# Optimization experiments

Measured on AMD Instinct MI355X. Metric: run time of the kernel, lower is better.

Reference implementation:

```python
import jax, jax.numpy as jnp
import numpy as np

KS = 5
NF = 64
B, H, W = 2, 160, 160


def _conv1x1(x, w, b):
    # x: (B,Ci,H,W), w: (Co,Ci)
    return jnp.einsum('oi,bihw->bohw', w, x) + b[None, :, None, None]


def _conv2x2(x, w, b, dil):
    # x: (B,1,Hp,Wp), w: (64,1,2,2); VALID conv with dilation dil
    y = jax.lax.conv_general_dilated(x, w, (1, 1), 'VALID',
                                     rhs_dilation=(dil, dil),
                                     dimension_numbers=('NCHW', 'OIHW', 'NCHW'))
    return y + b[None, :, None, None]


def _conv_s(x, w, b):
    # conv1 module, mode 's': gather taps (0,0),(1,1),(1,2),(2,1) of each 3x3 patch,
    # then (1,4) conv == linear combo of 4 shifted images.
    h = x.shape[2] - 2
    wd = x.shape[3] - 2
    x0 = x[:, 0]
    taps = jnp.stack([x0[:, 0:h, 0:wd],
                      x0[:, 1:h + 1, 1:wd + 1],
                      x0[:, 1:h + 1, 2:wd + 2],
                      x0[:, 2:h + 2, 1:wd + 1]], axis=1)  # (B,4,h,wd)
    return jnp.einsum('ok,bkhw->bohw', w.reshape(NF, 4), taps) + b[None, :, None, None]


def _construct(c, dense_ps):
    # relu then dense 1x1-conv chain with channel concat, final 1x1 -> 4 channels
    x = jax.nn.relu(c)
    for (wt, bs) in dense_ps[:-1]:
        feat = jax.nn.relu(_conv1x1(x, wt, bs))
        x = jnp.concatenate([x, feat], axis=1)
    wt, bs = dense_ps[-1]
    return _conv1x1(x, wt, bs)


def _ag(x, sigx, sigy, theta, sigr):
    # x: (B,ks,ks,HW); params: (B,HW). Per-pixel anisotropic bilateral kernel.
    ks = x.shape[1]
    r = jnp.arange(ks, dtype=x.dtype) - ks // 2
    sq = (r[:, None] ** 2 + r[None, :] ** 2)[None, :, :, None]  # (1,ks,ks,1)
    sx = sigx[:, None, None, :]
    sy = sigy[:, None, None, :]
    th = theta[:, None, None, :]
    sr = sigr[:, None, None, :]
    spatial = jnp.exp(-sq / (2.0 * sr ** 2))
    disx = jnp.abs(x[:, ks // 2:ks // 2 + 1] - x)       # center row
    disy = jnp.abs(x[:, :, ks // 2:ks // 2 + 1] - x)    # center col
    a = sx * disx
    bb = sy * disy
    color = jnp.exp(-0.5 * (a ** 2 - 2.0 * th * a * bb + bb ** 2))
    kern = spatial * color
    kern = kern / jnp.sum(kern, axis=(1, 2), keepdims=True)
    return jnp.sum(kern * x, axis=(1, 2))  # (B,HW)


def _forward(x_in, conv1x_w, conv1x_b, conv1c_w, conv1c_b, conv1cs_w, conv1cs_b,
             w2, b2, w3, b3, w4, b4, w5, b5, w6, b6):
    dense_ps = [(w2, b2), (w3, b3), (w4, b4), (w5, b5), (w6, b6)]

    def fk(x, mod):
        if mod == 's':
            c = _conv_s(x, conv1cs_w, conv1cs_b)
        elif mod == 'c':
            c = _conv2x2(x, conv1c_w, conv1c_b, 2)
        else:
            c = _conv2x2(x, conv1x_w, conv1x_b, 1)
        return _construct(c, dense_ps)

    def mode_ens(x, p, mod):
        pad = lambda z: jnp.pad(z, ((0, 0), (0, 0), (0, p), (0, p)), mode='reflect')
        r0 = fk(pad(x), mod)
        r2 = jnp.rot90(fk(pad(jnp.rot90(x, 2, (2, 3))), mod), 2, (2, 3))
        r1 = jnp.rot90(fk(pad(jnp.rot90(x, 1, (2, 3))), mod), 3, (2, 3))
        r3 = jnp.rot90(fk(pad(jnp.rot90(x, 3, (2, 3))), mod), 1, (2, 3))
        return (r0 + r2) / 2.0, (r1 + r3) / 2.0

    e1x, e2x = mode_ens(x_in, 1, 'x')
    e1s, e2s = mode_ens(x_in, 2, 's')
    e1c, e2c = mode_ens(x_in, 2, 'c')
    par = (e1x + e2x + e1s + e2s + e1c + e2c) / 6.0  # (B,4,H,W)

    b, c, h, w = x_in.shape
    sigx = jnp.clip(jax.nn.sigmoid(par[:, 0]).reshape(b, -1) + 1e-6, 0.0, 1.0)
    sigy = jnp.clip(jax.nn.sigmoid(par[:, 1]).reshape(b, -1) + 1e-6, 0.0, 1.0)
    theta = jnp.clip(jnp.tanh(par[:, 2]).reshape(b, -1), -1.0, 1.0)
    sigr = jnp.clip(jnp.tanh(par[:, 3]).reshape(b, -1) + 1e-6, -1.0, 1.0)

    ph = KS // 2
    xt = jnp.pad(x_in, ((0, 0), (0, 0), (ph, ph), (ph, ph)))  # zero pad
    # unfold -> (B, KS, KS, H*W)
    patches = jnp.stack([jnp.stack([xt[:, 0, i:i + h, j:j + w].reshape(b, -1)
                                    for j in range(KS)], axis=1)
                         for i in range(KS)], axis=1)
    outs = _ag(patches, sigx * 20.0, sigy * 20.0, theta, sigr * 10.0 + 10.0).reshape(b, c, h, w)
    return outs, sigx, sigy, theta, sigr


def setup_inputs() -> dict:
    key = jax.random.key(0)
    k = jax.random.split(key, 10)
    def kn(kk, shape, fan_in):
        return jax.random.normal(kk, shape, jnp.float32) * np.float32(np.sqrt(2.0 / fan_in))
    zb = lambda n: jnp.zeros((n,), jnp.float32)
    return {
        'x_in': jax.random.normal(k[0], (B, 1, H, W), jnp.float32),
        'conv1x_w': kn(k[1], (NF, 1, 2, 2), 4), 'conv1x_b': zb(NF),
        'conv1c_w': kn(k[2], (NF, 1, 2, 2), 4), 'conv1c_b': zb(NF),
        'conv1cs_w': kn(k[3], (NF, 1, 1, 4), 4), 'conv1cs_b': zb(NF),
        'w2': kn(k[4], (NF, NF), NF), 'b2': zb(NF),
        'w3': kn(k[5], (NF, 2 * NF), 2 * NF), 'b3': zb(NF),
        'w4': kn(k[6], (NF, 3 * NF), 3 * NF), 'b4': zb(NF),
        'w5': kn(k[7], (NF, 4 * NF), 4 * NF), 'b5': zb(NF),
        'w6': kn(k[8], (4, 5 * NF), 5 * NF), 'b6': zb(4),
    }


def reference(x_in, conv1x_w, conv1x_b, conv1c_w, conv1c_b, conv1cs_w, conv1cs_b,
              w2, b2, w3, b3, w4, b4, w5, b5, w6, b6):
    return _forward(x_in, conv1x_w, conv1x_b, conv1c_w, conv1c_b, conv1cs_w, conv1cs_b,
                    w2, b2, w3, b3, w4, b4, w5, b5, w6, b6)
```

## Files before the change

kernel.cpp:

```cpp
#include <hip/hip_runtime.h>
#include <hip/hip_bf16.h>
#include <math.h>
#include <string.h>


#define NN   160
#define NPIX 25600

typedef __attribute__((ext_vector_type(4))) float float4v;
typedef __attribute__((ext_vector_type(8))) unsigned short ushort8;
typedef __attribute__((ext_vector_type(2))) unsigned int uint2v;
typedef __attribute__((ext_vector_type(4))) unsigned int uint4v;
typedef __attribute__((ext_vector_type(8))) __bf16 bf16x8;

__device__ __forceinline__ int refp(int a) { return (a <= NN - 1) ? a : (2 * (NN - 1) - a); }

__device__ __forceinline__ unsigned int pk2(float lo, float hi) {
    float2 f; f.x = lo; f.y = hi;
    __hip_bfloat162 h = __float22bfloat162_rn(f);
    unsigned int u;
    memcpy(&u, &h, 4);
    return u;
}
__device__ __forceinline__ ushort8 cvt8(const float* __restrict__ p) {
    const float4v f0 = *(const float4v*)p;
    const float4v f1 = *(const float4v*)(p + 4);
    uint4v u;
    u[0] = pk2(f0[0], f0[1]); u[1] = pk2(f0[2], f0[3]);
    u[2] = pk2(f1[0], f1[1]); u[3] = pk2(f1[2], f1[3]);
    return __builtin_bit_cast(ushort8, u);
}

template <int NCH>
__device__ __forceinline__ void dense_layer(const ushort8 (&A)[NCH], float4v biasv,
                                            unsigned short* Xs, int w, int lo16, int lq) {
    const int K = NCH * 32;
#pragma unroll
    for (int pp = 0; pp < 2; ++pp) {
        const int px0 = (pp * 2) * 16 + lo16;
        const int px1 = (pp * 2 + 1) * 16 + lo16;
        float4v acc0 = biasv, acc1 = biasv;
#pragma unroll
        for (int s = 0; s < NCH; ++s) {
            const int c8 = s * 4 + lq;
            const bf16x8 bf0 = __builtin_bit_cast(bf16x8, *(const ushort8*)&Xs[c8 * 512 + px0 * 8]);
            const bf16x8 bf1 = __builtin_bit_cast(bf16x8, *(const ushort8*)&Xs[c8 * 512 + px1 * 8]);
            const bf16x8 af  = __builtin_bit_cast(bf16x8, A[s]);
            acc0 = __builtin_amdgcn_mfma_f32_16x16x32_bf16(af, bf0, acc0, 0, 0, 0);
            acc1 = __builtin_amdgcn_mfma_f32_16x16x32_bf16(af, bf1, acc1, 0, 0, 0);
        }
        const int cb = K + w * 16 + lq * 4;
        uint2v o0, o1;
        o0[0] = pk2(fmaxf(acc0[0], 0.0f), fmaxf(acc0[1], 0.0f));
        o0[1] = pk2(fmaxf(acc0[2], 0.0f), fmaxf(acc0[3], 0.0f));
        o1[0] = pk2(fmaxf(acc1[0], 0.0f), fmaxf(acc1[1], 0.0f));
        o1[1] = pk2(fmaxf(acc1[2], 0.0f), fmaxf(acc1[3], 0.0f));
        *(uint2v*)&Xs[(cb >> 3) * 512 + px0 * 8 + (cb & 7)] = o0;
        *(uint2v*)&Xs[(cb >> 3) * 512 + px1 * 8 + (cb & 7)] = o1;
    }
    __syncthreads();
}

__global__ __launch_bounds__(256, 3) void bnet_mlp_kernel(
    const float* __restrict__ x,
    const float* __restrict__ wx, const float* __restrict__ bx,
    const float* __restrict__ wcs, const float* __restrict__ bcs,
    const float* __restrict__ wc, const float* __restrict__ bc,
    const float* __restrict__ w2, const float* __restrict__ b2,
    const float* __restrict__ w3, const float* __restrict__ b3,
    const float* __restrict__ w4, const float* __restrict__ b4,
    const float* __restrict__ w5, const float* __restrict__ b5,
    const float* __restrict__ w6,
    float* __restrict__ par)
{
    __shared__ unsigned short Xs[20480];
    float* red = (float*)Xs;

    const int t = threadIdx.x;
    const int lane = t & 63;
    const int lo16 = lane & 15;
    const int lq = lane >> 4;
    const int w = __builtin_amdgcn_readfirstlane(t >> 6);

    const int arow = w * 16 + lo16;
    ushort8 a2[2], a3[4], a4[6], a5[8], a6[3];
#pragma unroll
    for (int s = 0; s < 2; ++s) a2[s] = cvt8(&w2[arow * 64 + s * 32 + lq * 8]);
#pragma unroll
    for (int s = 0; s < 4; ++s) a3[s] = cvt8(&w3[arow * 128 + s * 32 + lq * 8]);
#pragma unroll
    for (int s = 0; s < 6; ++s) a4[s] = cvt8(&w4[arow * 192 + s * 32 + lq * 8]);
#pragma unroll
    for (int s = 0; s < 8; ++s) a5[s] = cvt8(&w5[arow * 256 + s * 32 + lq * 8]);
#pragma unroll
    for (int c = 0; c < 3; ++c) {
        const int ch = (3 * w + c) * 32;
        if (ch < 320 && lo16 < 4) {
            a6[c] = cvt8(&w6[lo16 * 320 + ch + lq * 8]);
        } else {
            ushort8 z = {0, 0, 0, 0, 0, 0, 0, 0};
            a6[c] = z;
        }
    }
    const float4v b2v = *(const float4v*)&b2[w * 16 + lq * 4];
    const float4v b3v = *(const float4v*)&b3[w * 16 + lq * 4];
    const float4v b4v = *(const float4v*)&b4[w * 16 + lq * 4];
    const float4v b5v = *(const float4v*)&b5[w * 16 + lq * 4];

    const int bid = blockIdx.x;
    const int nit = 12 + (bid < 384 ? 1 : 0);
    const int g0  = (bid < 384) ? bid * 13 : bid * 12 + 384;

    for (int it = 0; it < nit; ++it) {
        const int g = g0 + it;
        const int v = g % 12;
        const int tb = g / 12;
        const int tile = tb >> 1;
        const int b = tb & 1;
        const int mode = v >> 2;
        const int k = v & 3;

        const float* xb = x + b * NPIX;
        const float* w1 = (mode == 0) ? wx : (mode == 1) ? wcs : wc;
        const float* b1 = (mode == 0) ? bx : (mode == 1) ? bcs : bc;
        int DY[4], DX[4];
        if (mode == 0)      { DY[0]=0; DY[1]=0; DY[2]=1; DY[3]=1;  DX[0]=0; DX[1]=1; DX[2]=0; DX[3]=1; }
        else if (mode == 1) { DY[0]=0; DY[1]=1; DY[2]=1; DY[3]=2;  DX[0]=0; DX[1]=1; DX[2]=2; DX[3]=1; }
        else                { DY[0]=0; DY[1]=0; DY[2]=2; DY[3]=2;  DX[0]=0; DX[1]=2; DX[2]=0; DX[3]=2; }

        const int pix = tile * 64 + lane;
        const int pi = pix / NN;
        const int pj = pix - pi * NN;

        __syncthreads();

        float s4[4];
#pragma unroll
        for (int tt = 0; tt < 4; ++tt) {
            const int dy = DY[tt], dx = DX[tt];
            int r, c;
            if (k == 0)      { r = refp(pi + dy); c = refp(pj + dx); }
            else if (k == 1) { r = refp(pi + dx); c = (pj >= dy) ? (pj - dy) : (dy - pj); }
            else if (k == 2) { r = (pi >= dy) ? (pi - dy) : (dy - pi);
                               c = (pj >= dx) ? (pj - dx) : (dx - pj); }
            else             { r = (pi >= dx) ? (pi - dx) : (dx - pi); c = refp(pj + dy); }
            s4[tt] = xb[r * NN + c];
        }
        float co[16];
#pragma unroll
        for (int oo = 0; oo < 16; ++oo) {
            const int o = w * 16 + oo;
            float cacc = b1[o];
#pragma unroll
            for (int tt = 0; tt < 4; ++tt) cacc = fmaf(w1[o * 4 + tt], s4[tt], cacc);
            co[oo] = fmaxf(cacc, 0.0f);
        }
        uint4v pka, pkb;
#pragma unroll
        for (int q = 0; q < 4; ++q) {
            pka[q] = pk2(co[2 * q], co[2 * q + 1]);
            pkb[q] = pk2(co[8 + 2 * q], co[9 + 2 * q]);
        }
        *(uint4v*)&Xs[(w * 2) * 512 + lane * 8]     = pka;
        *(uint4v*)&Xs[(w * 2 + 1) * 512 + lane * 8] = pkb;
        __syncthreads();

        dense_layer<2>(a2, b2v, Xs, w, lo16, lq);
        dense_layer<4>(a3, b3v, Xs, w, lo16, lq);
        dense_layer<6>(a4, b4v, Xs, w, lo16, lq);
        dense_layer<8>(a5, b5v, Xs, w, lo16, lq);

        float4v acc6[4];
#pragma unroll
        for (int pt = 0; pt < 4; ++pt) { float4v z = {0.f, 0.f, 0.f, 0.f}; acc6[pt] = z; }
#pragma unroll
        for (int pt = 0; pt < 4; ++pt) {
            const int px = pt * 16 + lo16;
#pragma unroll
            for (int c = 0; c < 3; ++c) {
                int chb = (3 * w + c) * 32;
                chb = (chb < 288) ? chb : 288;
                const int c8 = (chb >> 3) + lq;
                const bf16x8 bf = __builtin_bit_cast(
                    bf16x8, *(const ushort8*)&Xs[c8 * 512 + px * 8]);
                const bf16x8 af = __builtin_bit_cast(bf16x8, a6[c]);
                acc6[pt] = __builtin_amdgcn_mfma_f32_16x16x32_bf16(af, bf, acc6[pt], 0, 0, 0);
            }
        }
        __syncthreads();

        if (lq == 0) {
#pragma unroll
            for (int pt = 0; pt < 4; ++pt)
                *(float4v*)&red[(((w * 4) + pt) * 16 + lo16) * 4] = acc6[pt];
        }
        __syncthreads();
        if (w == 0) {
            float4v sv;
#pragma unroll
            for (int r = 0; r < 4; ++r)
                sv[r] = red[(((0 * 4) + lq) * 16 + lo16) * 4 + r]
                      + red[(((1 * 4) + lq) * 16 + lo16) * 4 + r]
                      + red[(((2 * 4) + lq) * 16 + lo16) * 4 + r]
                      + red[(((3 * 4) + lq) * 16 + lo16) * 4 + r];
            const int pixg = tile * 64 + lq * 16 + lo16;
#pragma unroll
            for (int r = 0; r < 4; ++r)
                atomicAdd(&par[(r * 2 + b) * NPIX + pixg], sv[r]);
        }
    }
}

__global__ __launch_bounds__(256) void bnet_bilateral_kernel(
    const float* __restrict__ x, const float* __restrict__ b6,
    float* __restrict__ out)
{
    const int tid = blockIdx.x * 256 + threadIdx.x;
    const int b = tid / NPIX;
    const int pix = tid - b * NPIX;
    const int pi = pix / NN;
    const int pj = pix - pi * NN;

    float* par = out + 2 * NPIX;
    const float inv12 = 1.0f / 12.0f;
    const float p0 = par[(0 + b) * NPIX + pix] * inv12 + b6[0];
    const float p1 = par[(2 + b) * NPIX + pix] * inv12 + b6[1];
    const float p2 = par[(4 + b) * NPIX + pix] * inv12 + b6[2];
    const float p3 = par[(6 + b) * NPIX + pix] * inv12 + b6[3];

    float sigx = 1.0f / (1.0f + __expf(-p0)) + 1e-6f;
    sigx = fminf(fmaxf(sigx, 0.0f), 1.0f);
    float sigy = 1.0f / (1.0f + __expf(-p1)) + 1e-6f;
    sigy = fminf(fmaxf(sigy, 0.0f), 1.0f);
    float t2 = __expf(2.0f * fminf(fmaxf(p2, -15.0f), 15.0f));
    float th = (t2 - 1.0f) / (t2 + 1.0f);
    th = fminf(fmaxf(th, -1.0f), 1.0f);
    float t3 = __expf(2.0f * fminf(fmaxf(p3, -15.0f), 15.0f));
    float sigr = (t3 - 1.0f) / (t3 + 1.0f) + 1e-6f;
    sigr = fminf(fmaxf(sigr, -1.0f), 1.0f);

    par[(0 + b) * NPIX + pix] = sigx;
    par[(2 + b) * NPIX + pix] = sigy;
    par[(4 + b) * NPIX + pix] = th;
    par[(6 + b) * NPIX + pix] = sigr;

    const float sx = sigx * 20.0f;
    const float sy = sigy * 20.0f;
    const float sr = sigr * 10.0f + 10.0f;

    const float* xb = x + b * NPIX;
    float patch[5][5];
#pragma unroll
    for (int ky = 0; ky < 5; ++ky) {
#pragma unroll
        for (int kx = 0; kx < 5; ++kx) {
            const int r = pi + ky - 2, c = pj + kx - 2;
            patch[ky][kx] = (r >= 0 && r < NN && c >= 0 && c < NN) ? xb[r * NN + c] : 0.0f;
        }
    }

    const float inv2sr2 = 1.0f / (2.0f * sr * sr);
    float num = 0.0f, den = 0.0f;
#pragma unroll
    for (int ky = 0; ky < 5; ++ky) {
#pragma unroll
        for (int kx = 0; kx < 5; ++kx) {
            const float v = patch[ky][kx];
            const float dxv = fabsf(patch[2][kx] - v);
            const float dyv = fabsf(patch[ky][2] - v);
            const float a = sx * dxv;
            const float bb = sy * dyv;
            const float sq = (float)((ky - 2) * (ky - 2) + (kx - 2) * (kx - 2));
            const float kern = __expf(-sq * inv2sr2 - 0.5f * (a * a - 2.0f * th * a * bb + bb * bb));
            den += kern;
            num = fmaf(kern, v, num);
        }
    }
    out[tid] = num / den;
}

extern "C" void kernel_launch(void* const* d_in, const int* in_sizes, int n_in,
                              void* d_out, int out_size, void* d_ws, size_t ws_size,
                              hipStream_t stream) {
    const float* x   = (const float*)d_in[0];
    const float* wx  = (const float*)d_in[1];
    const float* bx  = (const float*)d_in[2];
    const float* wc  = (const float*)d_in[3];
    const float* bc  = (const float*)d_in[4];
    const float* wcs = (const float*)d_in[5];
    const float* bcs = (const float*)d_in[6];
    const float* w2  = (const float*)d_in[7];
    const float* b2  = (const float*)d_in[8];
    const float* w3  = (const float*)d_in[9];
    const float* b3  = (const float*)d_in[10];
    const float* w4  = (const float*)d_in[11];
    const float* b4  = (const float*)d_in[12];
    const float* w5  = (const float*)d_in[13];
    const float* b5  = (const float*)d_in[14];
    const float* w6  = (const float*)d_in[15];
    const float* b6  = (const float*)d_in[16];
    float* out = (float*)d_out;

    (void)hipMemsetAsync(out + 2 * NPIX, 0, 8 * NPIX * sizeof(float), stream);

    hipLaunchKernelGGL(bnet_mlp_kernel, dim3(768), dim3(256), 0, stream,
                       x, wx, bx, wcs, bcs, wc, bc,
                       w2, b2, w3, b3, w4, b4, w5, b5, w6,
                       out + 2 * NPIX);

    hipLaunchKernelGGL(bnet_bilateral_kernel, dim3(200), dim3(256), 0, stream,
                       x, b6, out);
}
```

Before: 179.5 us.

## Accumulate final-layer outputs across consecutive variants and rebalance grids

The MLP kernel now keeps the final 1x1 layer accumulators across consecutive work items that share the same tile/batch, flushing with a block reduction and atomics only when the tile changes, instead of after every variant. The grid grows to 1024 blocks with fewer items each and launch bounds ask for 4 blocks per CU. The bilateral kernel is relaunched with 64-thread blocks to spread across more CUs. Fewer atomics and barriers are traded against higher register pressure from the occupancy hint.

```diff
diff --git a/kernel.cpp b/kernel.cpp
--- a/kernel.cpp
+++ b/kernel.cpp
@@ -61,7 +61,7 @@
     __syncthreads();
 }
 
-__global__ __launch_bounds__(256, 3) void bnet_mlp_kernel(
+__global__ __launch_bounds__(256, 4) void bnet_mlp_kernel(
     const float* __restrict__ x,
     const float* __restrict__ wx, const float* __restrict__ bx,
     const float* __restrict__ wcs, const float* __restrict__ bcs,
@@ -108,8 +108,11 @@
     const float4v b5v = *(const float4v*)&b5[w * 16 + lq * 4];
 
     const int bid = blockIdx.x;
-    const int nit = 12 + (bid < 384 ? 1 : 0);
-    const int g0  = (bid < 384) ? bid * 13 : bid * 12 + 384;
+    const int nit = 9 + (bid < 384 ? 1 : 0);
+    const int g0  = (bid < 384) ? bid * 10 : bid * 9 + 384;
+
+    float4v acc6[4];
+    int cur_tb = -1;
 
     for (int it = 0; it < nit; ++it) {
         const int g = g0 + it;
@@ -120,6 +123,38 @@
         const int mode = v >> 2;
         const int k = v & 3;
 
+        __syncthreads();
+
+        if (tb != cur_tb) {
+            if (cur_tb >= 0) {
+                const int ftile = cur_tb >> 1;
+                const int fb = cur_tb & 1;
+                if (lq == 0) {
+#pragma unroll
+                    for (int pt = 0; pt < 4; ++pt)
+                        *(float4v*)&red[(((w * 4) + pt) * 16 + lo16) * 4] = acc6[pt];
+                }
+                __syncthreads();
+                if (w == 0) {
+                    float4v sv;
+#pragma unroll
+                    for (int r = 0; r < 4; ++r)
+                        sv[r] = red[(((0 * 4) + lq) * 16 + lo16) * 4 + r]
+                              + red[(((1 * 4) + lq) * 16 + lo16) * 4 + r]
+                              + red[(((2 * 4) + lq) * 16 + lo16) * 4 + r]
+                              + red[(((3 * 4) + lq) * 16 + lo16) * 4 + r];
+                    const int pixg = ftile * 64 + lq * 16 + lo16;
+#pragma unroll
+                    for (int r = 0; r < 4; ++r)
+                        atomicAdd(&par[(r * 2 + fb) * NPIX + pixg], sv[r]);
+                }
+                __syncthreads();
+            }
+#pragma unroll
+            for (int pt = 0; pt < 4; ++pt) { float4v z = {0.f, 0.f, 0.f, 0.f}; acc6[pt] = z; }
+            cur_tb = tb;
+        }
+
         const float* xb = x + b * NPIX;
         const float* w1 = (mode == 0) ? wx : (mode == 1) ? wcs : wc;
         const float* b1 = (mode == 0) ? bx : (mode == 1) ? bcs : bc;
@@ -131,8 +166,6 @@
         const int pix = tile * 64 + lane;
         const int pi = pix / NN;
         const int pj = pix - pi * NN;
-
-        __syncthreads();
 
         float s4[4];
 #pragma unroll
@@ -170,9 +203,6 @@
         dense_layer<6>(a4, b4v, Xs, w, lo16, lq);
         dense_layer<8>(a5, b5v, Xs, w, lo16, lq);
 
-        float4v acc6[4];
-#pragma unroll
-        for (int pt = 0; pt < 4; ++pt) { float4v z = {0.f, 0.f, 0.f, 0.f}; acc6[pt] = z; }
 #pragma unroll
         for (int pt = 0; pt < 4; ++pt) {
             const int px = pt * 16 + lo16;
@@ -187,8 +217,12 @@
                 acc6[pt] = __builtin_amdgcn_mfma_f32_16x16x32_bf16(af, bf, acc6[pt], 0, 0, 0);
             }
         }
-        __syncthreads();
-
+    }
+
+    __syncthreads();
+    {
+        const int ftile = cur_tb >> 1;
+        const int fb = cur_tb & 1;
         if (lq == 0) {
 #pragma unroll
             for (int pt = 0; pt < 4; ++pt)
@@ -203,19 +237,19 @@
                       + red[(((1 * 4) + lq) * 16 + lo16) * 4 + r]
                       + red[(((2 * 4) + lq) * 16 + lo16) * 4 + r]
                       + red[(((3 * 4) + lq) * 16 + lo16) * 4 + r];
-            const int pixg = tile * 64 + lq * 16 + lo16;
+            const int pixg = ftile * 64 + lq * 16 + lo16;
 #pragma unroll
             for (int r = 0; r < 4; ++r)
-                atomicAdd(&par[(r * 2 + b) * NPIX + pixg], sv[r]);
-        }
-    }
-}
-
-__global__ __launch_bounds__(256) void bnet_bilateral_kernel(
+                atomicAdd(&par[(r * 2 + fb) * NPIX + pixg], sv[r]);
+        }
+    }
+}
+
+__global__ __launch_bounds__(64) void bnet_bilateral_kernel(
     const float* __restrict__ x, const float* __restrict__ b6,
     float* __restrict__ out)
 {
-    const int tid = blockIdx.x * 256 + threadIdx.x;
+    const int tid = blockIdx.x * 64 + threadIdx.x;
     const int b = tid / NPIX;
     const int pix = tid - b * NPIX;
     const int pi = pix / NN;
@@ -303,11 +337,11 @@
 
     (void)hipMemsetAsync(out + 2 * NPIX, 0, 8 * NPIX * sizeof(float), stream);
 
-    hipLaunchKernelGGL(bnet_mlp_kernel, dim3(768), dim3(256), 0, stream,
+    hipLaunchKernelGGL(bnet_mlp_kernel, dim3(1024), dim3(256), 0, stream,
                        x, wx, bx, wcs, bcs, wc, bc,
                        w2, b2, w3, b3, w4, b4, w5, b5, w6,
                        out + 2 * NPIX);
 
-    hipLaunchKernelGGL(bnet_bilateral_kernel, dim3(200), dim3(256), 0, stream,
+    hipLaunchKernelGGL(bnet_bilateral_kernel, dim3(800), dim3(64), 0, stream,
                        x, b6, out);
 }
```

Result: slower. 203.6 us (+13.4%).

## Fuse MLP and bilateral filter into one kernel with per-tile accumulation

Applied to the files above, without the earlier changes.

Each block now owns one 64-pixel tile and runs all 12 variants itself, accumulating the final 1x1 conv in registers. This removes the global atomics, the memset and the separate bilateral launch. The parameter activation and the 5x5 bilateral filter run inside the same block, with four lanes per pixel and a shuffle reduction. Grid changes from 768 load-balanced blocks to 800 fixed blocks, and the conv1 weight and bias loads are vectorized. Register pinning asm is added to the weight fragments.

```diff
diff --git a/kernel.cpp b/kernel.cpp
--- a/kernel.cpp
+++ b/kernel.cpp
@@ -12,6 +12,8 @@
 typedef __attribute__((ext_vector_type(2))) unsigned int uint2v;
 typedef __attribute__((ext_vector_type(4))) unsigned int uint4v;
 typedef __attribute__((ext_vector_type(8))) __bf16 bf16x8;
+
+#define PINV(x) asm volatile("" : "+v"(x))
 
 __device__ __forceinline__ int refp(int a) { return (a <= NN - 1) ? a : (2 * (NN - 1) - a); }
 
@@ -61,7 +63,10 @@
     __syncthreads();
 }
 
-__global__ __launch_bounds__(256, 3) void bnet_mlp_kernel(
+__global__
+__attribute__((amdgpu_flat_work_group_size(256, 256)))
+__attribute__((amdgpu_waves_per_eu(3, 3)))
+void bnet_fused_kernel(
     const float* __restrict__ x,
     const float* __restrict__ wx, const float* __restrict__ bx,
     const float* __restrict__ wcs, const float* __restrict__ bcs,
@@ -70,8 +75,8 @@
     const float* __restrict__ w3, const float* __restrict__ b3,
     const float* __restrict__ w4, const float* __restrict__ b4,
     const float* __restrict__ w5, const float* __restrict__ b5,
-    const float* __restrict__ w6,
-    float* __restrict__ par)
+    const float* __restrict__ w6, const float* __restrict__ b6,
+    float* __restrict__ out)
 {
     __shared__ unsigned short Xs[20480];
     float* red = (float*)Xs;
@@ -85,13 +90,13 @@
     const int arow = w * 16 + lo16;
     ushort8 a2[2], a3[4], a4[6], a5[8], a6[3];
 #pragma unroll
-    for (int s = 0; s < 2; ++s) a2[s] = cvt8(&w2[arow * 64 + s * 32 + lq * 8]);
-#pragma unroll
-    for (int s = 0; s < 4; ++s) a3[s] = cvt8(&w3[arow * 128 + s * 32 + lq * 8]);
-#pragma unroll
-    for (int s = 0; s < 6; ++s) a4[s] = cvt8(&w4[arow * 192 + s * 32 + lq * 8]);
-#pragma unroll
-    for (int s = 0; s < 8; ++s) a5[s] = cvt8(&w5[arow * 256 + s * 32 + lq * 8]);
+    for (int s = 0; s < 2; ++s) { a2[s] = cvt8(&w2[arow * 64 + s * 32 + lq * 8]);  PINV(a2[s]); }
+#pragma unroll
+    for (int s = 0; s < 4; ++s) { a3[s] = cvt8(&w3[arow * 128 + s * 32 + lq * 8]); PINV(a3[s]); }
+#pragma unroll
+    for (int s = 0; s < 6; ++s) { a4[s] = cvt8(&w4[arow * 192 + s * 32 + lq * 8]); PINV(a4[s]); }
+#pragma unroll
+    for (int s = 0; s < 8; ++s) { a5[s] = cvt8(&w5[arow * 256 + s * 32 + lq * 8]); PINV(a5[s]); }
 #pragma unroll
     for (int c = 0; c < 3; ++c) {
         const int ch = (3 * w + c) * 32;
@@ -101,38 +106,38 @@
             ushort8 z = {0, 0, 0, 0, 0, 0, 0, 0};
             a6[c] = z;
         }
+        PINV(a6[c]);
     }
     const float4v b2v = *(const float4v*)&b2[w * 16 + lq * 4];
     const float4v b3v = *(const float4v*)&b3[w * 16 + lq * 4];
     const float4v b4v = *(const float4v*)&b4[w * 16 + lq * 4];
     const float4v b5v = *(const float4v*)&b5[w * 16 + lq * 4];
 
-    const int bid = blockIdx.x;
-    const int nit = 12 + (bid < 384 ? 1 : 0);
-    const int g0  = (bid < 384) ? bid * 13 : bid * 12 + 384;
-
-    for (int it = 0; it < nit; ++it) {
-        const int g = g0 + it;
-        const int v = g % 12;
-        const int tb = g / 12;
-        const int tile = tb >> 1;
-        const int b = tb & 1;
-        const int mode = v >> 2;
-        const int k = v & 3;
-
-        const float* xb = x + b * NPIX;
+    const int tb = blockIdx.x;
+    const int tile = tb >> 1;
+    const int b = tb & 1;
+    const float* xb = x + b * NPIX;
+
+    const int pix0 = tile * 64 + lane;
+    const int pi = pix0 / NN;
+    const int pj = pix0 - pi * NN;
+
+    float4v acc6[4];
+#pragma unroll
+    for (int pt = 0; pt < 4; ++pt) { float4v z = {0.f, 0.f, 0.f, 0.f}; acc6[pt] = z; }
+
+    for (int it = 0; it < 12; ++it) {
+        const int mode = it >> 2;
+        const int k = it & 3;
+
+        __syncthreads();
+
         const float* w1 = (mode == 0) ? wx : (mode == 1) ? wcs : wc;
         const float* b1 = (mode == 0) ? bx : (mode == 1) ? bcs : bc;
         int DY[4], DX[4];
         if (mode == 0)      { DY[0]=0; DY[1]=0; DY[2]=1; DY[3]=1;  DX[0]=0; DX[1]=1; DX[2]=0; DX[3]=1; }
         else if (mode == 1) { DY[0]=0; DY[1]=1; DY[2]=1; DY[3]=2;  DX[0]=0; DX[1]=1; DX[2]=2; DX[3]=1; }
         else                { DY[0]=0; DY[1]=0; DY[2]=2; DY[3]=2;  DX[0]=0; DX[1]=2; DX[2]=0; DX[3]=2; }
-
-        const int pix = tile * 64 + lane;
-        const int pi = pix / NN;
-        const int pj = pix - pi * NN;
-
-        __syncthreads();
 
         float s4[4];
 #pragma unroll
@@ -146,13 +151,17 @@
             else             { r = (pi >= dx) ? (pi - dx) : (dx - pi); c = refp(pj + dy); }
             s4[tt] = xb[r * NN + c];
         }
+        float4v b1v[4];
+#pragma unroll
+        for (int q = 0; q < 4; ++q) b1v[q] = *(const float4v*)&b1[w * 16 + q * 4];
         float co[16];
 #pragma unroll
         for (int oo = 0; oo < 16; ++oo) {
             const int o = w * 16 + oo;
-            float cacc = b1[o];
-#pragma unroll
-            for (int tt = 0; tt < 4; ++tt) cacc = fmaf(w1[o * 4 + tt], s4[tt], cacc);
+            const float4v wv = *(const float4v*)&w1[o * 4];
+            float cacc = b1v[oo >> 2][oo & 3];
+#pragma unroll
+            for (int tt = 0; tt < 4; ++tt) cacc = fmaf(wv[tt], s4[tt], cacc);
             co[oo] = fmaxf(cacc, 0.0f);
         }
         uint4v pka, pkb;
@@ -170,9 +179,6 @@
         dense_layer<6>(a4, b4v, Xs, w, lo16, lq);
         dense_layer<8>(a5, b5v, Xs, w, lo16, lq);
 
-        float4v acc6[4];
-#pragma unroll
-        for (int pt = 0; pt < 4; ++pt) { float4v z = {0.f, 0.f, 0.f, 0.f}; acc6[pt] = z; }
 #pragma unroll
         for (int pt = 0; pt < 4; ++pt) {
             const int px = pt * 16 + lo16;
@@ -183,100 +189,114 @@
                 const int c8 = (chb >> 3) + lq;
                 const bf16x8 bf = __builtin_bit_cast(
                     bf16x8, *(const ushort8*)&Xs[c8 * 512 + px * 8]);
-                const bf16x8 af = __builtin_bit_cast(bf16x8, a6[c]);
-                acc6[pt] = __builtin_amdgcn_mfma_f32_16x16x32_bf16(af, bf, acc6[pt], 0, 0, 0);
+                acc6[pt] = __builtin_amdgcn_mfma_f32_16x16x32_bf16(
+                    __builtin_bit_cast(bf16x8, a6[c]), bf, acc6[pt], 0, 0, 0);
             }
         }
-        __syncthreads();
-
-        if (lq == 0) {
-#pragma unroll
-            for (int pt = 0; pt < 4; ++pt)
-                *(float4v*)&red[(((w * 4) + pt) * 16 + lo16) * 4] = acc6[pt];
-        }
-        __syncthreads();
-        if (w == 0) {
-            float4v sv;
-#pragma unroll
-            for (int r = 0; r < 4; ++r)
-                sv[r] = red[(((0 * 4) + lq) * 16 + lo16) * 4 + r]
-                      + red[(((1 * 4) + lq) * 16 + lo16) * 4 + r]
-                      + red[(((2 * 4) + lq) * 16 + lo16) * 4 + r]
-                      + red[(((3 * 4) + lq) * 16 + lo16) * 4 + r];
-            const int pixg = tile * 64 + lq * 16 + lo16;
-#pragma unroll
-            for (int r = 0; r < 4; ++r)
-                atomicAdd(&par[(r * 2 + b) * NPIX + pixg], sv[r]);
-        }
-    }
-}
-
-__global__ __launch_bounds__(256) void bnet_bilateral_kernel(
-    const float* __restrict__ x, const float* __restrict__ b6,
-    float* __restrict__ out)
-{
-    const int tid = blockIdx.x * 256 + threadIdx.x;
-    const int b = tid / NPIX;
-    const int pix = tid - b * NPIX;
-    const int pi = pix / NN;
-    const int pj = pix - pi * NN;
+    }
 
     float* par = out + 2 * NPIX;
-    const float inv12 = 1.0f / 12.0f;
-    const float p0 = par[(0 + b) * NPIX + pix] * inv12 + b6[0];
-    const float p1 = par[(2 + b) * NPIX + pix] * inv12 + b6[1];
-    const float p2 = par[(4 + b) * NPIX + pix] * inv12 + b6[2];
-    const float p3 = par[(6 + b) * NPIX + pix] * inv12 + b6[3];
-
-    float sigx = 1.0f / (1.0f + __expf(-p0)) + 1e-6f;
-    sigx = fminf(fmaxf(sigx, 0.0f), 1.0f);
-    float sigy = 1.0f / (1.0f + __expf(-p1)) + 1e-6f;
-    sigy = fminf(fmaxf(sigy, 0.0f), 1.0f);
-    float t2 = __expf(2.0f * fminf(fmaxf(p2, -15.0f), 15.0f));
-    float th = (t2 - 1.0f) / (t2 + 1.0f);
-    th = fminf(fmaxf(th, -1.0f), 1.0f);
-    float t3 = __expf(2.0f * fminf(fmaxf(p3, -15.0f), 15.0f));
-    float sigr = (t3 - 1.0f) / (t3 + 1.0f) + 1e-6f;
-    sigr = fminf(fmaxf(sigr, -1.0f), 1.0f);
-
-    par[(0 + b) * NPIX + pix] = sigx;
-    par[(2 + b) * NPIX + pix] = sigy;
-    par[(4 + b) * NPIX + pix] = th;
-    par[(6 + b) * NPIX + pix] = sigr;
-
-    const float sx = sigx * 20.0f;
-    const float sy = sigy * 20.0f;
-    const float sr = sigr * 10.0f + 10.0f;
-
-    const float* xb = x + b * NPIX;
-    float patch[5][5];
-#pragma unroll
-    for (int ky = 0; ky < 5; ++ky) {
+    __syncthreads();
+
+    if (lq == 0) {
+#pragma unroll
+        for (int pt = 0; pt < 4; ++pt)
+            *(float4v*)&red[(((w * 4) + pt) * 16 + lo16) * 4] = acc6[pt];
+    }
+    __syncthreads();
+
+    if (w == 0) {
+        float4v sv;
+#pragma unroll
+        for (int r = 0; r < 4; ++r)
+            sv[r] = red[(((0 * 4) + lq) * 16 + lo16) * 4 + r]
+                  + red[(((1 * 4) + lq) * 16 + lo16) * 4 + r]
+                  + red[(((2 * 4) + lq) * 16 + lo16) * 4 + r]
+                  + red[(((3 * 4) + lq) * 16 + lo16) * 4 + r];
+        const float inv12 = 1.0f / 12.0f;
+        const float p0 = sv[0] * inv12 + b6[0];
+        const float p1 = sv[1] * inv12 + b6[1];
+        const float p2 = sv[2] * inv12 + b6[2];
+        const float p3 = sv[3] * inv12 + b6[3];
+
+        float sigx = 1.0f / (1.0f + __expf(-p0)) + 1e-6f;
+        sigx = fminf(fmaxf(sigx, 0.0f), 1.0f);
+        float sigy = 1.0f / (1.0f + __expf(-p1)) + 1e-6f;
+        sigy = fminf(fmaxf(sigy, 0.0f), 1.0f);
+        float t2 = __expf(2.0f * fminf(fmaxf(p2, -15.0f), 15.0f));
+        float th = (t2 - 1.0f) / (t2 + 1.0f);
+        th = fminf(fmaxf(th, -1.0f), 1.0f);
+        float t3 = __expf(2.0f * fminf(fmaxf(p3, -15.0f), 15.0f));
+        float sigr = (t3 - 1.0f) / (t3 + 1.0f) + 1e-6f;
+        sigr = fminf(fmaxf(sigr, -1.0f), 1.0f);
+
+        const int pixg = tile * 64 + lane;
+        par[(0 + b) * NPIX + pixg] = sigx;
+        par[(2 + b) * NPIX + pixg] = sigy;
+        par[(4 + b) * NPIX + pixg] = th;
+        par[(6 + b) * NPIX + pixg] = sigr;
+
+        red[lane * 4 + 0] = sigx;
+        red[lane * 4 + 1] = sigy;
+        red[lane * 4 + 2] = th;
+        red[lane * 4 + 3] = sigr;
+    }
+    __syncthreads();
+
+    {
+        const int pxl = w * 16 + (lane >> 2);
+        const int sub = lane & 3;
+        const int pix = tile * 64 + pxl;
+        const int bpi = pix / NN;
+        const int bpj = pix - bpi * NN;
+
+        const float sigx = red[pxl * 4 + 0];
+        const float sigy = red[pxl * 4 + 1];
+        const float th   = red[pxl * 4 + 2];
+        const float sigr = red[pxl * 4 + 3];
+        const float sx = sigx * 20.0f;
+        const float sy = sigy * 20.0f;
+        const float sr = sigr * 10.0f + 10.0f;
+        const float inv2sr2 = 1.0f / (2.0f * sr * sr);
+
+        float v2[5];
 #pragma unroll
         for (int kx = 0; kx < 5; ++kx) {
-            const int r = pi + ky - 2, c = pj + kx - 2;
-            patch[ky][kx] = (r >= 0 && r < NN && c >= 0 && c < NN) ? xb[r * NN + c] : 0.0f;
-        }
-    }
-
-    const float inv2sr2 = 1.0f / (2.0f * sr * sr);
-    float num = 0.0f, den = 0.0f;
-#pragma unroll
-    for (int ky = 0; ky < 5; ++ky) {
-#pragma unroll
-        for (int kx = 0; kx < 5; ++kx) {
-            const float v = patch[ky][kx];
-            const float dxv = fabsf(patch[2][kx] - v);
-            const float dyv = fabsf(patch[ky][2] - v);
-            const float a = sx * dxv;
-            const float bb = sy * dyv;
-            const float sq = (float)((ky - 2) * (ky - 2) + (kx - 2) * (kx - 2));
-            const float kern = __expf(-sq * inv2sr2 - 0.5f * (a * a - 2.0f * th * a * bb + bb * bb));
-            den += kern;
-            num = fmaf(kern, v, num);
-        }
-    }
-    out[tid] = num / den;
+            const int c = bpj + kx - 2;
+            v2[kx] = (c >= 0 && c < NN) ? xb[bpi * NN + c] : 0.0f;
+        }
+
+        float num = 0.0f, den = 0.0f;
+#pragma unroll
+        for (int q = 0; q < 2; ++q) {
+            const int ky = (q == 0) ? sub : 4;
+            if (q == 1 && sub != 0) break;
+            const int r = bpi + ky - 2;
+            const bool rin = (r >= 0 && r < NN);
+            float rowv[5];
+#pragma unroll
+            for (int kx = 0; kx < 5; ++kx) {
+                const int c = bpj + kx - 2;
+                rowv[kx] = (rin && c >= 0 && c < NN) ? xb[r * NN + c] : 0.0f;
+            }
+            const float vc = rowv[2];
+#pragma unroll
+            for (int kx = 0; kx < 5; ++kx) {
+                const float v = rowv[kx];
+                const float dxv = fabsf(v2[kx] - v);
+                const float dyv = fabsf(vc - v);
+                const float a = sx * dxv;
+                const float bb = sy * dyv;
+                const float sq = (float)((ky - 2) * (ky - 2) + (kx - 2) * (kx - 2));
+                const float kern = __expf(-sq * inv2sr2 - 0.5f * (a * a - 2.0f * th * a * bb + bb * bb));
+                den += kern;
+                num = fmaf(kern, v, num);
+            }
+        }
+        num += __shfl_xor(num, 1); den += __shfl_xor(den, 1);
+        num += __shfl_xor(num, 2); den += __shfl_xor(den, 2);
+        if (sub == 0) out[b * NPIX + pix] = num / den;
+    }
 }
 
 extern "C" void kernel_launch(void* const* d_in, const int* in_sizes, int n_in,
@@ -301,13 +321,8 @@
     const float* b6  = (const float*)d_in[16];
     float* out = (float*)d_out;
 
-    (void)hipMemsetAsync(out + 2 * NPIX, 0, 8 * NPIX * sizeof(float), stream);
-
-    hipLaunchKernelGGL(bnet_mlp_kernel, dim3(768), dim3(256), 0, stream,
+    hipLaunchKernelGGL(bnet_fused_kernel, dim3(800), dim3(256), 0, stream,
                        x, wx, bx, wcs, bcs, wc, bc,
-                       w2, b2, w3, b3, w4, b4, w5, b5, w6,
-                       out + 2 * NPIX);
-
-    hipLaunchKernelGGL(bnet_bilateral_kernel, dim3(200), dim3(256), 0, stream,
-                       x, b6, out);
-}
+                       w2, b2, w3, b3, w4, b4, w5, b5, w6, b6,
+                       out);
+}
```

After: 197.5 us. 10.0% more time.
